# Kernel optimization log

Measured on AMD Instinct MI355X. Metric: run time of the kernel, lower is better.

The kernel has to match this reference:

```python
import jax, jax.numpy as jnp
import numpy as np

N = 500_000   # number of tree nodes
L = 16        # number of labels
K = 4         # tree arity


def setup_inputs() -> dict:
    key = jax.random.key(0)
    k1, k2, k3, k4 = jax.random.split(key, 4)
    unary_potentials = jax.random.normal(k1, (N, L), dtype=jnp.float32)
    edge_potentials = jax.random.normal(k2, (N, L, L), dtype=jnp.float32)
    beliefs = jax.random.normal(k3, (N, L), dtype=jnp.float32)
    true_labels = jax.random.randint(k4, (N,), 0, L, dtype=jnp.int32)
    # K-ary tree: node i (i>=1) has parent (i-1)//K; node 0 is root
    child_idx = jnp.arange(1, N, dtype=jnp.int32)
    parent_idx = (child_idx - 1) // K
    # internal nodes = keys of children_dict (nodes that have children)
    internal_mask = jnp.zeros((N,), dtype=bool).at[parent_idx].set(True)
    return {
        "unary_potentials": unary_potentials,
        "edge_potentials": edge_potentials,
        "beliefs": beliefs,
        "true_labels": true_labels,
        "parent_idx": parent_idx,
        "child_idx": child_idx,
        "internal_mask": internal_mask,
    }


def reference(unary_potentials, edge_potentials, beliefs, true_labels,
              parent_idx, child_idx, internal_mask):
    # partition function from the root belief vector
    z = jax.scipy.special.logsumexp(beliefs[0])

    # unary potential at each node's true label: [N]
    node_unary = jnp.take_along_axis(unary_potentials, true_labels[:, None], axis=1)[:, 0]

    # loop `for parent in children_dict`: unary for every internal node
    pot = jnp.sum(jnp.where(internal_mask, node_unary, 0.0))

    # loop over children: edge potential edge_potentials[child][i][j]
    pi = true_labels[parent_idx]   # parent true label per edge
    ci = true_labels[child_idx]    # child true label per edge
    pot = pot + jnp.sum(edge_potentials[child_idx, pi, ci])

    # `if child not in children_dict`: unary for leaf children only
    leaf_child = ~internal_mask[child_idx]
    pot = pot + jnp.sum(jnp.where(leaf_child, node_unary[child_idx], 0.0))

    return -(pot - z)
```

## Files before the change

### kernel.cpp

```cpp
#include <hip/hip_runtime.h>


#define NBLK 2048
#define NTHR 256

__global__ __launch_bounds__(NTHR) void tree_crf_partial(
    const float* __restrict__ U,
    const float* __restrict__ E,
    const int* __restrict__ tl,
    float* __restrict__ partials,
    int N)
{
    int tid = blockIdx.x * NTHR + threadIdx.x;
    int stride = NBLK * NTHR;
    float acc = 0.0f;
    for (int i = tid; i < N; i += stride) {
        int l = tl[i];
        acc += U[(long)i * 16 + l];
        if (i >= 1) {
            int p = tl[(i - 1) >> 2];
            acc += E[((long)i << 8) + p * 16 + l];
        }
    }
    #pragma unroll
    for (int off = 32; off > 0; off >>= 1)
        acc += __shfl_down(acc, off, 64);
    __shared__ float s[NTHR / 64];
    int lane = threadIdx.x & 63;
    int wave = threadIdx.x >> 6;
    if (lane == 0) s[wave] = acc;
    __syncthreads();
    if (threadIdx.x == 0) {
        float v = 0.0f;
        #pragma unroll
        for (int w = 0; w < NTHR / 64; ++w) v += s[w];
        partials[blockIdx.x] = v;
    }
}

__global__ __launch_bounds__(NTHR) void tree_crf_finalize(
    const float* __restrict__ beliefs,
    const float* __restrict__ partials,
    float* __restrict__ out)
{
    float acc = 0.0f;
    for (int i = threadIdx.x; i < NBLK; i += NTHR)
        acc += partials[i];
    #pragma unroll
    for (int off = 32; off > 0; off >>= 1)
        acc += __shfl_down(acc, off, 64);
    __shared__ float s[NTHR / 64];
    int lane = threadIdx.x & 63;
    int wave = threadIdx.x >> 6;
    if (lane == 0) s[wave] = acc;
    __syncthreads();
    if (threadIdx.x == 0) {
        float pot = 0.0f;
        #pragma unroll
        for (int w = 0; w < NTHR / 64; ++w) pot += s[w];
        float m = beliefs[0];
        #pragma unroll
        for (int j = 1; j < 16; ++j) m = fmaxf(m, beliefs[j]);
        float se = 0.0f;
        #pragma unroll
        for (int j = 0; j < 16; ++j) se += __expf(beliefs[j] - m);
        float z = m + __logf(se);
        out[0] = z - pot;
    }
}

extern "C" void kernel_launch(void* const* d_in, const int* in_sizes, int n_in,
                              void* d_out, int out_size, void* d_ws, size_t ws_size,
                              hipStream_t stream) {
    const float* U       = (const float*)d_in[0];
    const float* E       = (const float*)d_in[1];
    const float* beliefs = (const float*)d_in[2];
    const int*   tl      = (const int*)d_in[3];
    int N = in_sizes[3];

    float* partials = (float*)d_ws;
    float* out      = (float*)d_out;

    tree_crf_partial<<<NBLK, NTHR, 0, stream>>>(U, E, tl, partials, N);
    tree_crf_finalize<<<1, NTHR, 0, stream>>>(beliefs, partials, out);
}
```

Baseline: 24.21 us.

## Process four sibling nodes per thread with vectorized label loads and nontemporal gathers

Each thread now handles four consecutive nodes, which share one parent, so their labels come from a single int4 load and the parent label is read once. The grid is sized to cover all nodes in one pass instead of a fixed 2048-block grid-stride loop. Gathers into U and E use nontemporal loads to avoid polluting cache. Each thread issues eight independent gathers for more memory-level parallelism, but there are more blocks, so the finalize kernel reduces about 489 partials instead of 2048.

```diff
diff --git a/kernel.cpp b/kernel.cpp
--- a/kernel.cpp
+++ b/kernel.cpp
@@ -1,7 +1,6 @@
 #include <hip/hip_runtime.h>
 
 
-#define NBLK 2048
 #define NTHR 256
 
 __global__ __launch_bounds__(NTHR) void tree_crf_partial(
@@ -11,23 +10,46 @@
     float* __restrict__ partials,
     int N)
 {
-    int tid = blockIdx.x * NTHR + threadIdx.x;
-    int stride = NBLK * NTHR;
+    const int tid = blockIdx.x * NTHR + threadIdx.x;
+    const int Nq  = N >> 2;
     float acc = 0.0f;
-    for (int i = tid; i < N; i += stride) {
-        int l = tl[i];
-        acc += U[(long)i * 16 + l];
-        if (i >= 1) {
-            int p = tl[(i - 1) >> 2];
-            acc += E[((long)i << 8) + p * 16 + l];
+
+    if (tid < Nq) {
+        const int base = tid << 2;
+        const int4 l4 = *reinterpret_cast<const int4*>(tl + base);
+        const int plB = tl[tid];
+        const int plA = (tid > 0) ? tl[tid - 1] : 0;
+
+        float u0 = __builtin_nontemporal_load(&U[((size_t)base + 0) * 16 + l4.x]);
+        float u1 = __builtin_nontemporal_load(&U[((size_t)base + 1) * 16 + l4.y]);
+        float u2 = __builtin_nontemporal_load(&U[((size_t)base + 2) * 16 + l4.z]);
+        float u3 = __builtin_nontemporal_load(&U[((size_t)base + 3) * 16 + l4.w]);
+
+        float e0 = 0.0f;
+        if (tid > 0)
+            e0 = __builtin_nontemporal_load(&E[(((size_t)base + 0) << 8) + plA * 16 + l4.x]);
+        float e1 = __builtin_nontemporal_load(&E[(((size_t)base + 1) << 8) + plB * 16 + l4.y]);
+        float e2 = __builtin_nontemporal_load(&E[(((size_t)base + 2) << 8) + plB * 16 + l4.z]);
+        float e3 = __builtin_nontemporal_load(&E[(((size_t)base + 3) << 8) + plB * 16 + l4.w]);
+
+        acc = ((u0 + u1) + (u2 + u3)) + ((e0 + e1) + (e2 + e3));
+    } else if (tid == Nq && (N & 3)) {
+        for (int n = Nq << 2; n < N; ++n) {
+            int l = tl[n];
+            acc += U[(size_t)n * 16 + l];
+            if (n >= 1) {
+                int p = tl[(n - 1) >> 2];
+                acc += E[((size_t)n << 8) + p * 16 + l];
+            }
         }
     }
+
     #pragma unroll
     for (int off = 32; off > 0; off >>= 1)
         acc += __shfl_down(acc, off, 64);
     __shared__ float s[NTHR / 64];
-    int lane = threadIdx.x & 63;
-    int wave = threadIdx.x >> 6;
+    const int lane = threadIdx.x & 63;
+    const int wave = threadIdx.x >> 6;
     if (lane == 0) s[wave] = acc;
     __syncthreads();
     if (threadIdx.x == 0) {
@@ -41,17 +63,18 @@
 __global__ __launch_bounds__(NTHR) void tree_crf_finalize(
     const float* __restrict__ beliefs,
     const float* __restrict__ partials,
-    float* __restrict__ out)
+    float* __restrict__ out,
+    int nb)
 {
     float acc = 0.0f;
-    for (int i = threadIdx.x; i < NBLK; i += NTHR)
+    for (int i = threadIdx.x; i < nb; i += NTHR)
         acc += partials[i];
     #pragma unroll
     for (int off = 32; off > 0; off >>= 1)
         acc += __shfl_down(acc, off, 64);
     __shared__ float s[NTHR / 64];
-    int lane = threadIdx.x & 63;
-    int wave = threadIdx.x >> 6;
+    const int lane = threadIdx.x & 63;
+    const int wave = threadIdx.x >> 6;
     if (lane == 0) s[wave] = acc;
     __syncthreads();
     if (threadIdx.x == 0) {
@@ -76,11 +99,15 @@
     const float* E       = (const float*)d_in[1];
     const float* beliefs = (const float*)d_in[2];
     const int*   tl      = (const int*)d_in[3];
-    int N = in_sizes[3];
+    const int N = in_sizes[3];
+
+    const int Nq = N >> 2;
+    const int threads_needed = Nq + ((N & 3) ? 1 : 0);
+    const int nb = (threads_needed + NTHR - 1) / NTHR;
 
     float* partials = (float*)d_ws;
     float* out      = (float*)d_out;
 
-    tree_crf_partial<<<NBLK, NTHR, 0, stream>>>(U, E, tl, partials, N);
-    tree_crf_finalize<<<1, NTHR, 0, stream>>>(beliefs, partials, out);
+    tree_crf_partial<<<nb, NTHR, 0, stream>>>(U, E, tl, partials, N);
+    tree_crf_finalize<<<1, NTHR, 0, stream>>>(beliefs, partials, out, nb);
 }
```

Measured after the change: 21.42 us. 11.5% less time.

## Fuse partial and final reduction via last-block atomic counter, two nodes per thread

Applied to the files above, without the earlier changes.

Merges the two kernels into one: each block writes its partial sum, bumps an atomic counter, and the last block to finish reduces all partials and computes the logsumexp result. Each thread now handles two adjacent nodes with a vectorized label load and nontemporal gathers, and the grid is sized from N instead of a fixed grid-stride loop. This removes the second kernel launch but adds a memset launch, and the larger grid means more blocks contend on the counter.

```diff
diff --git a/kernel.cpp b/kernel.cpp
--- a/kernel.cpp
+++ b/kernel.cpp
@@ -1,71 +1,92 @@
 #include <hip/hip_runtime.h>
 
 
-#define NBLK 2048
 #define NTHR 256
 
-__global__ __launch_bounds__(NTHR) void tree_crf_partial(
+__device__ __forceinline__ float nt_load(const float* p) {
+    return __builtin_nontemporal_load(p);
+}
+
+__global__ __launch_bounds__(NTHR) void tree_crf_fused(
     const float* __restrict__ U,
     const float* __restrict__ E,
-    const int* __restrict__ tl,
+    const float* __restrict__ beliefs,
+    const int*   __restrict__ tl,
+    float* __restrict__ out,
     float* __restrict__ partials,
+    unsigned int* __restrict__ counter,
     int N)
 {
-    int tid = blockIdx.x * NTHR + threadIdx.x;
-    int stride = NBLK * NTHR;
+    const int tid = blockIdx.x * NTHR + threadIdx.x;
+    const int n0  = tid << 1;
     float acc = 0.0f;
-    for (int i = tid; i < N; i += stride) {
-        int l = tl[i];
-        acc += U[(long)i * 16 + l];
-        if (i >= 1) {
-            int p = tl[(i - 1) >> 2];
-            acc += E[((long)i << 8) + p * 16 + l];
-        }
+
+    if (n0 + 1 < N) {
+        const int n1 = n0 + 1;
+        const int2 l2 = *reinterpret_cast<const int2*>(tl + n0);
+        const int p1 = tl[n0 >> 2];
+        const int p0 = (n0 >= 1) ? tl[(n0 - 1) >> 2] : 0;
+
+        const float u0 = nt_load(&U[((size_t)n0 << 4) + l2.x]);
+        const float u1 = nt_load(&U[((size_t)n1 << 4) + l2.y]);
+        const float e1 = nt_load(&E[((size_t)n1 << 8) + p1 * 16 + l2.y]);
+        float e0 = 0.0f;
+        if (n0 >= 1)
+            e0 = nt_load(&E[((size_t)n0 << 8) + p0 * 16 + l2.x]);
+        acc = (u0 + u1) + (e0 + e1);
+    } else if (n0 < N) {
+        const int l = tl[n0];
+        acc = U[((size_t)n0 << 4) + l];
+        if (n0 >= 1)
+            acc += E[((size_t)n0 << 8) + tl[(n0 - 1) >> 2] * 16 + l];
     }
+
     #pragma unroll
     for (int off = 32; off > 0; off >>= 1)
         acc += __shfl_down(acc, off, 64);
     __shared__ float s[NTHR / 64];
-    int lane = threadIdx.x & 63;
-    int wave = threadIdx.x >> 6;
+    __shared__ int is_last;
+    const int lane = threadIdx.x & 63;
+    const int wave = threadIdx.x >> 6;
     if (lane == 0) s[wave] = acc;
     __syncthreads();
+
     if (threadIdx.x == 0) {
         float v = 0.0f;
         #pragma unroll
         for (int w = 0; w < NTHR / 64; ++w) v += s[w];
-        partials[blockIdx.x] = v;
+        __hip_atomic_store(&partials[blockIdx.x], v, __ATOMIC_RELAXED,
+                           __HIP_MEMORY_SCOPE_AGENT);
+        __threadfence();
+        unsigned int old = __hip_atomic_fetch_add(counter, 1u, __ATOMIC_ACQ_REL,
+                                                  __HIP_MEMORY_SCOPE_AGENT);
+        is_last = (old == gridDim.x - 1) ? 1 : 0;
     }
-}
+    __syncthreads();
 
-__global__ __launch_bounds__(NTHR) void tree_crf_finalize(
-    const float* __restrict__ beliefs,
-    const float* __restrict__ partials,
-    float* __restrict__ out)
-{
-    float acc = 0.0f;
-    for (int i = threadIdx.x; i < NBLK; i += NTHR)
-        acc += partials[i];
-    #pragma unroll
-    for (int off = 32; off > 0; off >>= 1)
-        acc += __shfl_down(acc, off, 64);
-    __shared__ float s[NTHR / 64];
-    int lane = threadIdx.x & 63;
-    int wave = threadIdx.x >> 6;
-    if (lane == 0) s[wave] = acc;
-    __syncthreads();
-    if (threadIdx.x == 0) {
-        float pot = 0.0f;
+    if (is_last) {
+        float a = 0.0f;
+        for (unsigned int i = threadIdx.x; i < gridDim.x; i += NTHR)
+            a += __hip_atomic_load(&partials[i], __ATOMIC_RELAXED,
+                                   __HIP_MEMORY_SCOPE_AGENT);
         #pragma unroll
-        for (int w = 0; w < NTHR / 64; ++w) pot += s[w];
-        float m = beliefs[0];
-        #pragma unroll
-        for (int j = 1; j < 16; ++j) m = fmaxf(m, beliefs[j]);
-        float se = 0.0f;
-        #pragma unroll
-        for (int j = 0; j < 16; ++j) se += __expf(beliefs[j] - m);
-        float z = m + __logf(se);
-        out[0] = z - pot;
+        for (int off = 32; off > 0; off >>= 1)
+            a += __shfl_down(a, off, 64);
+        if (lane == 0) s[wave] = a;
+        __syncthreads();
+        if (threadIdx.x == 0) {
+            float pot = 0.0f;
+            #pragma unroll
+            for (int w = 0; w < NTHR / 64; ++w) pot += s[w];
+            float m = beliefs[0];
+            #pragma unroll
+            for (int j = 1; j < 16; ++j) m = fmaxf(m, beliefs[j]);
+            float se = 0.0f;
+            #pragma unroll
+            for (int j = 0; j < 16; ++j) se += __expf(beliefs[j] - m);
+            const float z = m + __logf(se);
+            out[0] = z - pot;
+        }
     }
 }
 
@@ -76,11 +97,16 @@
     const float* E       = (const float*)d_in[1];
     const float* beliefs = (const float*)d_in[2];
     const int*   tl      = (const int*)d_in[3];
-    int N = in_sizes[3];
+    const int N = in_sizes[3];
 
-    float* partials = (float*)d_ws;
-    float* out      = (float*)d_out;
+    int nb = (N + 2 * NTHR - 1) / (2 * NTHR);
+    nb = ((nb + 255) / 256) * 256;
 
-    tree_crf_partial<<<NBLK, NTHR, 0, stream>>>(U, E, tl, partials, N);
-    tree_crf_finalize<<<1, NTHR, 0, stream>>>(beliefs, partials, out);
+    float* partials        = (float*)d_ws;
+    unsigned int* counter  = (unsigned int*)((char*)d_ws + (size_t)nb * sizeof(float));
+    float* out             = (float*)d_out;
+
+    hipMemsetAsync(counter, 0, sizeof(unsigned int), stream);
+    tree_crf_fused<<<nb, NTHR, 0, stream>>>(U, E, beliefs, tl, out,
+                                            partials, counter, N);
 }
```

Result: slower. 96.52 us (+298.6%).
